# Optimization experiments

Hardware: AMD Instinct MI355X
Metric: run time of the kernel (lower is better)

The kernel has to match this reference:

```python
import jax, jax.numpy as jnp
import numpy as np

EPS = 1e-5
NUM_HEADS = 16
NUM_KV_HEADS = 4
HEAD_DIM = 64
TOP_K = 2


def _layer_norm(x, w, b):
    m = jnp.mean(x, axis=-1, keepdims=True)
    v = jnp.mean((x - m) ** 2, axis=-1, keepdims=True)
    return (x - m) * jax.lax.rsqrt(v + EPS) * w + b


def setup_inputs() -> dict:
    key = jax.random.key(0)
    ks = jax.random.split(key, 8)
    S, B, H = 2048, 1, 1024
    E, F = 8, 4096
    q_per_kv = NUM_HEADS // NUM_KV_HEADS
    qkv_out = NUM_KV_HEADS * (q_per_kv + 2) * HEAD_DIM  # 1536

    def w(k, shape, scale=0.02):
        return jax.random.normal(k, shape, dtype=jnp.float32) * scale

    return {
        "hidden_states": jax.random.normal(ks[0], (S, B, H), dtype=jnp.float32),
        "ln1_weight": jnp.ones((H,), jnp.float32),
        "ln1_bias": jnp.zeros((H,), jnp.float32),
        "ln2_weight": jnp.ones((H,), jnp.float32),
        "ln2_bias": jnp.zeros((H,), jnp.float32),
        "qkv_weight": w(ks[1], (qkv_out, H)),
        "proj_weight": w(ks[2], (H, H)),
        "router_weight": w(ks[3], (H, E)),
        "moe_w1": w(ks[4], (E, H, F)),
        "moe_w2": w(ks[5], (E, F, H)),
    }


def reference(hidden_states, ln1_weight, ln1_bias, ln2_weight, ln2_bias,
              qkv_weight, proj_weight, router_weight, moe_w1, moe_w2):
    S, B, H = hidden_states.shape
    D = HEAD_DIM
    Hq, Hkv = NUM_HEADS, NUM_KV_HEADS
    g = Hq // Hkv                      # queries per kv head (GQA group)
    scale = 1.0 / np.sqrt(D)

    # ---- attention block ----
    ln1_out = _layer_norm(hidden_states, ln1_weight, ln1_bias)
    qkv = ln1_out @ qkv_weight.T                      # [S,B,Hkv*(g+2)*D]
    qkv = qkv.reshape(S, B, Hkv, (g + 2) * D)
    q = qkv[..., : g * D].reshape(S, B, Hq, D)        # [S,B,Hq,D]
    k = qkv[..., g * D : (g + 1) * D]                 # [S,B,Hkv,D]
    v = qkv[..., (g + 1) * D :]                       # [S,B,Hkv,D]

    # cp_size == 1 -> Ulysses all-to-alls are identity
    q_bf = q.transpose(1, 2, 0, 3).reshape(B, Hkv, g, S, D)  # [B,Hkv,g,S,D]
    k_bf = k.transpose(1, 2, 0, 3)                           # [B,Hkv,S,D]
    v_bf = v.transpose(1, 2, 0, 3)

    scores = jnp.einsum("bkgsd,bktd->bkgst", q_bf, k_bf) * scale
    causal = jnp.tril(jnp.ones((S, S), dtype=bool))
    scores = jnp.where(causal, scores, jnp.float32(-1e30))
    probs = jax.nn.softmax(scores, axis=-1)
    attn = jnp.einsum("bkgst,bktd->bkgsd", probs, v_bf)      # [B,Hkv,g,S,D]
    attn = attn.reshape(B, Hq, S, D).transpose(2, 0, 1, 3).reshape(S, B, Hq * D)

    proj_out = attn @ proj_weight.T
    hidden_after_attn = hidden_states + proj_out

    # ---- MoE block ----
    ln2_out = _layer_norm(hidden_after_attn, ln2_weight, ln2_bias)
    x = ln2_out.reshape(-1, H)                        # [T,H]
    T = x.shape[0]

    logits = x @ router_weight                        # [T,E] (fp32)
    rprobs = jax.nn.softmax(logits, axis=-1)
    top_p, top_i = jax.lax.top_k(rprobs, TOP_K)       # [T,k]
    top_p = top_p / jnp.sum(top_p, axis=-1, keepdims=True)

    # ep_size == 1: dispatch/sort/all-to-all are a pure permutation; compute
    # each expert densely over all tokens, then gather the routed outputs
    # (identical math to sort+grouped-GEMM+unsort).
    fc1 = jnp.einsum("th,ehf->etf", x, moe_w1)        # [E,T,F]
    act = jax.nn.gelu(fc1, approximate=False)
    y = jnp.einsum("etf,efh->eth", act, moe_w2)       # [E,T,H]

    tok = jnp.arange(T)[:, None]                      # [T,1]
    gathered = y[top_i, tok, :]                       # [T,k,H]
    moe_out = jnp.sum(gathered * top_p[..., None], axis=1)  # [T,H]

    return hidden_after_attn + moe_out.reshape(S, B, H)
```

## Files before the change

kernel.cpp:

```cpp
#include <hip/hip_runtime.h>
#include <cstdint>
#include <cstddef>

typedef unsigned short u16;
typedef __attribute__((ext_vector_type(8))) short bf16x8;
typedef __attribute__((ext_vector_type(4))) float f32x4;

#define MFMA16(a, b, c) __builtin_amdgcn_mfma_f32_16x16x32_bf16((a), (b), (c), 0, 0, 0)

__device__ __forceinline__ u16 f2bf(float f) {
  uint32_t u = __builtin_bit_cast(uint32_t, f);
  u += 0x7fffu + ((u >> 16) & 1u);
  return (u16)(u >> 16);
}
__device__ __forceinline__ float bf2f(u16 h) {
  uint32_t u = ((uint32_t)h) << 16;
  return __builtin_bit_cast(float, u);
}

__device__ __forceinline__ void gload_lds16(const void* g, void* l) {
  __builtin_amdgcn_global_load_lds(
      (const __attribute__((address_space(1))) uint32_t*)g,
      (__attribute__((address_space(3))) uint32_t*)l, 16, 0, 0);
}

template<bool WRITE_LO, bool WRITE_F32>
__launch_bounds__(256)
__global__ void ln_kernel(const float* __restrict__ in,
                          const float* __restrict__ w, const float* __restrict__ b,
                          u16* __restrict__ out_hi, u16* __restrict__ out_lo,
                          float* __restrict__ out_f32)
{
  int row = blockIdx.x;
  int tid = threadIdx.x;
  const float* x = in + (size_t)row * 1024;
  float4 v = *(const float4*)(x + tid * 4);
  float s  = v.x + v.y + v.z + v.w;
  float s2 = v.x*v.x + v.y*v.y + v.z*v.z + v.w*v.w;
  #pragma unroll
  for (int d = 1; d < 64; d <<= 1) { s += __shfl_xor(s, d); s2 += __shfl_xor(s2, d); }
  __shared__ float red[2][4];
  int wid = tid >> 6;
  if ((tid & 63) == 0) { red[0][wid] = s; red[1][wid] = s2; }
  __syncthreads();
  s  = red[0][0] + red[0][1] + red[0][2] + red[0][3];
  s2 = red[1][0] + red[1][1] + red[1][2] + red[1][3];
  float mean = s * (1.0f / 1024.0f);
  float var  = s2 * (1.0f / 1024.0f) - mean * mean;
  float rstd = rsqrtf(var + 1e-5f);
  float vv[4] = {v.x, v.y, v.z, v.w};
  #pragma unroll
  for (int j = 0; j < 4; ++j) {
    int c = tid * 4 + j;
    float y = (vv[j] - mean) * rstd * w[c] + b[c];
    size_t idx = (size_t)row * 1024 + c;
    u16 hb = f2bf(y);
    out_hi[idx] = hb;
    if (WRITE_LO)  out_lo[idx] = f2bf(y - bf2f(hb));
    if (WRITE_F32) out_f32[idx] = y;
  }
}

__global__ void convert_split_kernel(const float* __restrict__ in,
                                     u16* __restrict__ hi, u16* __restrict__ lo, int n4)
{
  int i = blockIdx.x * blockDim.x + threadIdx.x;
  if (i >= n4) return;
  float4 v = *(const float4*)(in + (size_t)i * 4);
  float a[4] = {v.x, v.y, v.z, v.w};
  u16 hh[4], ll[4];
  #pragma unroll
  for (int j = 0; j < 4; ++j) {
    hh[j] = f2bf(a[j]);
    ll[j] = f2bf(a[j] - bf2f(hh[j]));
  }
  uint2 hp, lp;
  hp.x = (uint32_t)hh[0] | ((uint32_t)hh[1] << 16);
  hp.y = (uint32_t)hh[2] | ((uint32_t)hh[3] << 16);
  lp.x = (uint32_t)ll[0] | ((uint32_t)ll[1] << 16);
  lp.y = (uint32_t)ll[2] | ((uint32_t)ll[3] << 16);
  *(uint2*)(hi + (size_t)i * 4) = hp;
  *(uint2*)(lo + (size_t)i * 4) = lp;
}

__global__ void transpose_convert_kernel(const float* __restrict__ in, u16* __restrict__ out,
                                         int R, int C)
{
  __shared__ float t[32][33];
  size_t ebase = (size_t)blockIdx.z * R * C;
  int c0 = blockIdx.x * 32, r0 = blockIdx.y * 32;
  int tx = threadIdx.x, ty = threadIdx.y;
  #pragma unroll
  for (int i = 0; i < 4; ++i)
    t[ty + 8*i][tx] = in[ebase + (size_t)(r0 + ty + 8*i) * C + (c0 + tx)];
  __syncthreads();
  #pragma unroll
  for (int i = 0; i < 4; ++i)
    out[ebase + (size_t)(c0 + ty + 8*i) * R + (r0 + tx)] = f2bf(t[tx][ty + 8*i]);
}

__global__ void vtrans_kernel(const u16* __restrict__ qkv, u16* __restrict__ vT)
{
  __shared__ u16 t[32][34];
  int kvh = blockIdx.z;
  int s0 = blockIdx.x * 32, d0 = blockIdx.y * 32;
  int tx = threadIdx.x, ty = threadIdx.y;
  #pragma unroll
  for (int i = 0; i < 4; ++i)
    t[ty + 8*i][tx] = qkv[(size_t)(s0 + ty + 8*i) * 1536 + kvh * 384 + 320 + d0 + tx];
  __syncthreads();
  #pragma unroll
  for (int i = 0; i < 4; ++i)
    vT[((size_t)kvh * 64 + d0 + ty + 8*i) * 2048 + (s0 + tx)] = t[tx][ty + 8*i];
}

template<int MODE, bool SPLIT>
__launch_bounds__(256, SPLIT ? 2 : 4)
__global__ void gemm_kernel(const u16* __restrict__ Ahi, const u16* __restrict__ Alo,
                            const u16* __restrict__ Bhi, const u16* __restrict__ Blo,
                            int N, int K,
                            u16* __restrict__ Cb_hi, u16* __restrict__ Cb_lo,
                            float* __restrict__ Cf, const float* __restrict__ resid,
                            const int* __restrict__ tok_of_pair,
                            const int* __restrict__ counts, const int* __restrict__ prefix)
{
  int bn = blockIdx.x, bm = blockIdx.y;
  int row_base = 0;
  int count = 1 << 30;
  int kbeg = 0, kend = K;
  if constexpr (MODE >= 2) {
    int e = blockIdx.z;
    count = counts[e];
    if (bm * 128 >= count) return;
    row_base = prefix[e];
    Bhi += (size_t)e * N * K;
  }
  if constexpr (MODE == 3) {
    int s = bn >> 3;
    bn &= 7;
    int kc = K >> 2;
    kbeg = s * kc; kend = kbeg + kc;
    Cf += (size_t)s * 4096 * 1024;
  }
  __shared__ u16 As[2][SPLIT ? 2 : 1][128 * 32];
  __shared__ u16 Bs[2][SPLIT ? 2 : 1][128 * 32];

  int tid = threadIdx.x;
  int lane = tid & 63;
  int lo16 = lane & 15, hi4 = lane >> 4;
  int wid = tid >> 6, wr = wid >> 1, wc = wid & 1;

  const u16* gA[2][2];
  const u16* gB[2][2];
  int eidx[2];
  #pragma unroll
  for (int q = 0; q < 2; ++q) {
    int el = (q * 256 + tid) * 8;
    int r = el >> 5, c = el & 31;
    eidx[q] = el;
    if constexpr (MODE == 2) {
      int lim = count - bm * 128 - 1;
      int lr = r < lim ? r : lim;
      int token = tok_of_pair[row_base + bm * 128 + lr];
      gA[q][0] = Ahi + (size_t)token * K + c;
    } else if constexpr (MODE == 3) {
      int lim = count - bm * 128 - 1;
      int lr = r < lim ? r : lim;
      gA[q][0] = Ahi + (size_t)(row_base + bm * 128 + lr) * K + c;
    } else {
      gA[q][0] = Ahi + (size_t)(bm * 128 + r) * K + c;
      if constexpr (SPLIT) gA[q][1] = Alo + (size_t)(bm * 128 + r) * K + c;
    }
    gB[q][0] = Bhi + (size_t)(bn * 128 + r) * K + c;
    if constexpr (SPLIT) gB[q][1] = Blo + (size_t)(bn * 128 + r) * K + c;
  }

  auto stage = [&](int buf, int k0) {
    #pragma unroll
    for (int q = 0; q < 2; ++q) {
      gload_lds16(gA[q][0] + k0, &As[buf][0][eidx[q]]);
      gload_lds16(gB[q][0] + k0, &Bs[buf][0][eidx[q]]);
      if constexpr (SPLIT) {
        gload_lds16(gA[q][1] + k0, &As[buf][1][eidx[q]]);
        gload_lds16(gB[q][1] + k0, &Bs[buf][1][eidx[q]]);
      }
    }
  };

  const f32x4 zf = {0.f, 0.f, 0.f, 0.f};
  f32x4 acc[4][4];
  #pragma unroll
  for (int m = 0; m < 4; ++m)
    #pragma unroll
    for (int n = 0; n < 4; ++n) acc[m][n] = zf;

  stage(0, kbeg);
  __syncthreads();

  int cur = 0;
  for (int k0 = kbeg; k0 < kend; k0 += 32, cur ^= 1) {
    if (k0 + 32 < kend) stage(cur ^ 1, k0 + 32);

    bf16x8 a0[4], b0[4], a1[4], b1[4];
    #pragma unroll
    for (int m = 0; m < 4; ++m)
      a0[m] = *(const bf16x8*)&As[cur][0][(wr * 64 + m * 16 + lo16) * 32 + hi4 * 8];
    #pragma unroll
    for (int n = 0; n < 4; ++n)
      b0[n] = *(const bf16x8*)&Bs[cur][0][(wc * 64 + n * 16 + lo16) * 32 + hi4 * 8];
    if constexpr (SPLIT) {
      #pragma unroll
      for (int m = 0; m < 4; ++m)
        a1[m] = *(const bf16x8*)&As[cur][1][(wr * 64 + m * 16 + lo16) * 32 + hi4 * 8];
      #pragma unroll
      for (int n = 0; n < 4; ++n)
        b1[n] = *(const bf16x8*)&Bs[cur][1][(wc * 64 + n * 16 + lo16) * 32 + hi4 * 8];
    }
    #pragma unroll
    for (int m = 0; m < 4; ++m)
      #pragma unroll
      for (int n = 0; n < 4; ++n) {
        acc[m][n] = MFMA16(a0[m], b0[n], acc[m][n]);
        if constexpr (SPLIT) {
          acc[m][n] = MFMA16(a0[m], b1[n], acc[m][n]);
          acc[m][n] = MFMA16(a1[m], b0[n], acc[m][n]);
        }
      }
    __syncthreads();
  }

  #pragma unroll
  for (int m = 0; m < 4; ++m)
    #pragma unroll
    for (int n = 0; n < 4; ++n)
      #pragma unroll
      for (int r = 0; r < 4; ++r) {
        int lr = wr * 64 + m * 16 + hi4 * 4 + r;
        int col = bn * 128 + wc * 64 + n * 16 + lo16;
        float v = acc[m][n][r];
        if constexpr (MODE == 0) {
          size_t idx = (size_t)(bm * 128 + lr) * N + col;
          u16 hb = f2bf(v);
          Cb_hi[idx] = hb;
          Cb_lo[idx] = f2bf(v - bf2f(hb));
        } else if constexpr (MODE == 1) {
          size_t idx = (size_t)(bm * 128 + lr) * N + col;
          Cf[idx] = v + resid[idx];
        } else if constexpr (MODE == 2) {
          if (bm * 128 + lr < count) {
            size_t idx = (size_t)(row_base + bm * 128 + lr) * N + col;
            float g = 0.5f * v * (1.0f + erff(v * 0.70710678118654752f));
            Cb_hi[idx] = f2bf(g);
          }
        } else {
          if (bm * 128 + lr < count) {
            size_t idx = (size_t)(row_base + bm * 128 + lr) * N + col;
            Cf[idx] = v;
          }
        }
      }
}

__launch_bounds__(256)
__global__ void attn_kernel(const u16* __restrict__ qkv_hi, const u16* __restrict__ qkv_lo,
                            const u16* __restrict__ vT_hi, const u16* __restrict__ vT_lo,
                            u16* __restrict__ out_hi, u16* __restrict__ out_lo)
{
  int qb = (int)(gridDim.x - 1 - blockIdx.x);
  int h = blockIdx.y;
  int kvh = h >> 2, gi = h & 3;
  int tid = threadIdx.x;
  int lane = tid & 63;
  int w = tid >> 6;
  int lo16 = lane & 15, hi4 = lane >> 4;
  int q0w = qb * 64 + w * 16;
  int qoff = kvh * 384 + gi * 64;
  int koff = kvh * 384 + 256;

  __shared__ u16 Ks[2][64 * 64];
  __shared__ u16 Vs[2][64 * 64];
  __shared__ u16 Ps[2][4][16 * 72];

  bf16x8 qf[2][2];
  {
    const u16* ph = qkv_hi + (size_t)(q0w + lo16) * 1536 + qoff + hi4 * 8;
    const u16* pl = qkv_lo + (size_t)(q0w + lo16) * 1536 + qoff + hi4 * 8;
    qf[0][0] = *(const bf16x8*)ph;  qf[0][1] = *(const bf16x8*)(ph + 32);
    qf[1][0] = *(const bf16x8*)pl;  qf[1][1] = *(const bf16x8*)(pl + 32);
  }

  const f32x4 zf = {0.f, 0.f, 0.f, 0.f};
  float m_r[4], l_r[4];
  f32x4 o[4];
  #pragma unroll
  for (int r = 0; r < 4; ++r) { m_r[r] = -INFINITY; l_r[r] = 0.f; }
  #pragma unroll
  for (int n = 0; n < 4; ++n) o[n] = zf;

  int qrow[4];
  #pragma unroll
  for (int r = 0; r < 4; ++r) qrow[r] = q0w + hi4 * 4 + r;

  for (int t = 0; t <= qb; ++t) {
    int kv0 = t * 64;
    __syncthreads();
    #pragma unroll
    for (int it = 0; it < 2; ++it) {
      int u = it * 256 + tid;
      int row = u >> 3, ch = u & 7;
      int d = ((ch ^ (row & 7))) * 8;
      *(uint4*)&Ks[0][row * 64 + d] = *(const uint4*)(qkv_hi + (size_t)(kv0 + row) * 1536 + koff + ch * 8);
      *(uint4*)&Ks[1][row * 64 + d] = *(const uint4*)(qkv_lo + (size_t)(kv0 + row) * 1536 + koff + ch * 8);
      *(uint4*)&Vs[0][row * 64 + d] = *(const uint4*)(vT_hi + ((size_t)kvh * 64 + row) * 2048 + kv0 + ch * 8);
      *(uint4*)&Vs[1][row * 64 + d] = *(const uint4*)(vT_lo + ((size_t)kvh * 64 + row) * 2048 + kv0 + ch * 8);
    }
    __syncthreads();

    f32x4 sc[4];
    #pragma unroll
    for (int c2 = 0; c2 < 4; ++c2) {
      sc[c2] = zf;
      int krow = c2 * 16 + lo16;
      const u16* kb  = &Ks[0][krow * 64];
      const u16* kbl = &Ks[1][krow * 64];
      bf16x8 kh0 = *(const bf16x8*)&kb [((hi4    ) ^ (krow & 7)) * 8];
      bf16x8 kh1 = *(const bf16x8*)&kb [((hi4 + 4) ^ (krow & 7)) * 8];
      bf16x8 kl0 = *(const bf16x8*)&kbl[((hi4    ) ^ (krow & 7)) * 8];
      bf16x8 kl1 = *(const bf16x8*)&kbl[((hi4 + 4) ^ (krow & 7)) * 8];
      sc[c2] = MFMA16(qf[0][0], kh0, sc[c2]);
      sc[c2] = MFMA16(qf[0][1], kh1, sc[c2]);
      sc[c2] = MFMA16(qf[0][0], kl0, sc[c2]);
      sc[c2] = MFMA16(qf[0][1], kl1, sc[c2]);
      sc[c2] = MFMA16(qf[1][0], kh0, sc[c2]);
      sc[c2] = MFMA16(qf[1][1], kh1, sc[c2]);
    }

    float tmax[4] = {-INFINITY, -INFINITY, -INFINITY, -INFINITY};
    #pragma unroll
    for (int c2 = 0; c2 < 4; ++c2) {
      int kv = kv0 + c2 * 16 + lo16;
      #pragma unroll
      for (int r = 0; r < 4; ++r) {
        float sv = sc[c2][r] * 0.125f;
        if (kv > qrow[r]) sv = -1e30f;
        sc[c2][r] = sv;
        tmax[r] = fmaxf(tmax[r], sv);
      }
    }
    #pragma unroll
    for (int d = 1; d < 16; d <<= 1)
      #pragma unroll
      for (int r = 0; r < 4; ++r)
        tmax[r] = fmaxf(tmax[r], __shfl_xor(tmax[r], d));
    float rs[4], rowsum[4];
    #pragma unroll
    for (int r = 0; r < 4; ++r) {
      float mn = fmaxf(m_r[r], tmax[r]);
      rs[r] = __expf(m_r[r] - mn);
      m_r[r] = mn;
      rowsum[r] = 0.f;
    }
    #pragma unroll
    for (int c2 = 0; c2 < 4; ++c2)
      #pragma unroll
      for (int r = 0; r < 4; ++r) {
        float pv = __expf(sc[c2][r] - m_r[r]);
        sc[c2][r] = pv;
        rowsum[r] += pv;
      }
    #pragma unroll
    for (int d = 1; d < 16; d <<= 1)
      #pragma unroll
      for (int r = 0; r < 4; ++r)
        rowsum[r] += __shfl_xor(rowsum[r], d);
    #pragma unroll
    for (int r = 0; r < 4; ++r) l_r[r] = l_r[r] * rs[r] + rowsum[r];
    #pragma unroll
    for (int n = 0; n < 4; ++n)
      #pragma unroll
      for (int r = 0; r < 4; ++r) o[n][r] *= rs[r];

    #pragma unroll
    for (int c2 = 0; c2 < 4; ++c2)
      #pragma unroll
      for (int r = 0; r < 4; ++r) {
        float pv = sc[c2][r];
        u16 ph = f2bf(pv);
        int pidx = (hi4 * 4 + r) * 72 + c2 * 16 + lo16;
        Ps[0][w][pidx] = ph;
        Ps[1][w][pidx] = f2bf(pv - bf2f(ph));
      }
    __syncthreads();

    #pragma unroll
    for (int k2 = 0; k2 < 2; ++k2) {
      bf16x8 pah = *(const bf16x8*)&Ps[0][w][lo16 * 72 + k2 * 32 + hi4 * 8];
      bf16x8 pal = *(const bf16x8*)&Ps[1][w][lo16 * 72 + k2 * 32 + hi4 * 8];
      #pragma unroll
      for (int n = 0; n < 4; ++n) {
        int vrow = n * 16 + lo16;
        bf16x8 vh = *(const bf16x8*)&Vs[0][vrow * 64 + (((k2 * 4 + hi4) ^ (vrow & 7))) * 8];
        bf16x8 vl = *(const bf16x8*)&Vs[1][vrow * 64 + (((k2 * 4 + hi4) ^ (vrow & 7))) * 8];
        o[n] = MFMA16(pah, vh, o[n]);
        o[n] = MFMA16(pah, vl, o[n]);
        o[n] = MFMA16(pal, vh, o[n]);
      }
    }
  }

  #pragma unroll
  for (int n = 0; n < 4; ++n)
    #pragma unroll
    for (int r = 0; r < 4; ++r) {
      float v = o[n][r] / l_r[r];
      size_t idx = (size_t)(q0w + hi4 * 4 + r) * 1024 + h * 64 + n * 16 + lo16;
      u16 hb = f2bf(v);
      out_hi[idx] = hb;
      out_lo[idx] = f2bf(v - bf2f(hb));
    }
}

__launch_bounds__(64)
__global__ void router_kernel(const float* __restrict__ x, const float* __restrict__ rw,
                              int* __restrict__ counts, int* __restrict__ esel,
                              int* __restrict__ slotsel, float* __restrict__ wsel)
{
  int t = blockIdx.x;
  int l = threadIdx.x;
  float acc[8] = {0.f, 0.f, 0.f, 0.f, 0.f, 0.f, 0.f, 0.f};
  const float* xr = x + (size_t)t * 1024;
  for (int hh = l; hh < 1024; hh += 64) {
    float xv = xr[hh];
    const float* wp = rw + hh * 8;
    #pragma unroll
    for (int e = 0; e < 8; ++e) acc[e] = fmaf(xv, wp[e], acc[e]);
  }
  #pragma unroll
  for (int e = 0; e < 8; ++e)
    #pragma unroll
    for (int d = 1; d < 64; d <<= 1) acc[e] += __shfl_xor(acc[e], d);
  if (l == 0) {
    int e1 = 0;
    #pragma unroll
    for (int e = 1; e < 8; ++e) if (acc[e] > acc[e1]) e1 = e;
    int e2 = -1;
    #pragma unroll
    for (int e = 0; e < 8; ++e) {
      if (e == e1) continue;
      if (e2 < 0 || acc[e] > acc[e2]) e2 = e;
    }
    float p1 = 1.0f / (1.0f + expf(acc[e2] - acc[e1]));
    float p2 = 1.0f - p1;
    int s1 = atomicAdd(&counts[e1], 1);
    int s2 = atomicAdd(&counts[e2], 1);
    esel[t * 2] = e1; esel[t * 2 + 1] = e2;
    slotsel[t * 2] = s1; slotsel[t * 2 + 1] = s2;
    wsel[t * 2] = p1; wsel[t * 2 + 1] = p2;
  }
}

__global__ void build_lists_kernel(const int* __restrict__ counts, int* __restrict__ prefix,
                                   const int* __restrict__ esel, const int* __restrict__ slotsel,
                                   int* __restrict__ tok_of_pair, int* __restrict__ pair_idx)
{
  __shared__ int pfx[8];
  if (threadIdx.x == 0) {
    int a = 0;
    for (int e = 0; e < 8; ++e) { pfx[e] = a; prefix[e] = a; a += counts[e]; }
  }
  __syncthreads();
  for (int t = threadIdx.x; t < 2048; t += 256) {
    #pragma unroll
    for (int k = 0; k < 2; ++k) {
      int e = esel[t * 2 + k];
      int row = pfx[e] + slotsel[t * 2 + k];
      tok_of_pair[row] = t;
      pair_idx[t * 2 + k] = row;
    }
  }
}

__launch_bounds__(256)
__global__ void final_kernel(const float* __restrict__ hattn, const float* __restrict__ y,
                             const int* __restrict__ pair_idx, const float* __restrict__ wsel,
                             float* __restrict__ out)
{
  int t = blockIdx.x;
  int c = threadIdx.x * 4;
  int p0 = pair_idx[t * 2], p1 = pair_idx[t * 2 + 1];
  float w0 = wsel[t * 2], w1 = wsel[t * 2 + 1];
  float4 a = *(const float4*)(hattn + (size_t)t * 1024 + c);
  float y0x = 0.f, y0y = 0.f, y0z = 0.f, y0w = 0.f;
  float y1x = 0.f, y1y = 0.f, y1z = 0.f, y1w = 0.f;
  #pragma unroll
  for (int s = 0; s < 4; ++s) {
    const float* base = y + (size_t)s * 4096 * 1024;
    float4 v0 = *(const float4*)(base + (size_t)p0 * 1024 + c);
    float4 v1 = *(const float4*)(base + (size_t)p1 * 1024 + c);
    y0x += v0.x; y0y += v0.y; y0z += v0.z; y0w += v0.w;
    y1x += v1.x; y1y += v1.y; y1z += v1.z; y1w += v1.w;
  }
  float4 r;
  r.x = a.x + w0 * y0x + w1 * y1x;
  r.y = a.y + w0 * y0y + w1 * y1y;
  r.z = a.z + w0 * y0z + w1 * y1z;
  r.w = a.w + w0 * y0w + w1 * y1w;
  *(float4*)(out + (size_t)t * 1024 + c) = r;
}

extern "C" void kernel_launch(void* const* d_in, const int* in_sizes, int n_in,
                              void* d_out, int out_size, void* d_ws, size_t ws_size,
                              hipStream_t stream)
{
  const float* hidden   = (const float*)d_in[0];
  const float* ln1_w    = (const float*)d_in[1];
  const float* ln1_b    = (const float*)d_in[2];
  const float* ln2_w    = (const float*)d_in[3];
  const float* ln2_b    = (const float*)d_in[4];
  const float* qkv_w    = (const float*)d_in[5];
  const float* proj_w   = (const float*)d_in[6];
  const float* router_w = (const float*)d_in[7];
  const float* moe_w1   = (const float*)d_in[8];
  const float* moe_w2   = (const float*)d_in[9];
  float* out = (float*)d_out;

  char* ws = (char*)d_ws;
  size_t off = 0;
  auto alloc = [&](size_t bytes) -> void* {
    void* p = (void*)(ws + off);
    off += (bytes + 255) & ~(size_t)255;
    return p;
  };

  u16* wT      = (u16*)alloc(8ull * 4096 * 1024 * 2);
  float* hattn = (float*)alloc(2048ull * 1024 * 4);
  u16* x_hi    = (u16*)alloc(2048ull * 1024 * 2);
  u16* act     = (u16*)alloc(4096ull * 4096 * 2);
  float* ybuf  = (float*)alloc(4ull * 4096 * 1024 * 4);

  {
    char* ov = (char*)ybuf;
    size_t oo = 0;
    auto oalloc = [&](size_t bytes) -> void* {
      void* p = (void*)(ov + oo);
      oo += (bytes + 255) & ~(size_t)255;
      return p;
    };
    (void)oalloc;
  }
  char* ov = (char*)ybuf;
  size_t oo = 0;
  auto oalloc = [&](size_t bytes) -> void* {
    void* p = (void*)(ov + oo);
    oo += (bytes + 255) & ~(size_t)255;
    return p;
  };
  u16* ln1_hi  = (u16*)oalloc(2048ull * 1024 * 2);
  u16* ln1_lo  = (u16*)oalloc(2048ull * 1024 * 2);
  u16* qw_hi   = (u16*)oalloc(1536ull * 1024 * 2);
  u16* qw_lo   = (u16*)oalloc(1536ull * 1024 * 2);
  u16* pw_hi   = (u16*)oalloc(1024ull * 1024 * 2);
  u16* pw_lo   = (u16*)oalloc(1024ull * 1024 * 2);
  u16* qkv_hi  = (u16*)oalloc(2048ull * 1536 * 2);
  u16* qkv_lo  = (u16*)oalloc(2048ull * 1536 * 2);
  u16* vt_hi   = (u16*)oalloc(4ull * 64 * 2048 * 2);
  u16* vt_lo   = (u16*)oalloc(4ull * 64 * 2048 * 2);
  u16* at_hi   = (u16*)oalloc(2048ull * 1024 * 2);
  u16* at_lo   = (u16*)oalloc(2048ull * 1024 * 2);
  float* x_f32 = (float*)oalloc(2048ull * 1024 * 4);

  int* counts  = (int*)alloc(8 * 4);
  int* prefix  = (int*)alloc(8 * 4);
  int* esel    = (int*)alloc(2048ull * 2 * 4);
  int* slotsel = (int*)alloc(2048ull * 2 * 4);
  int* topair  = (int*)alloc(4096ull * 4);
  int* pairidx = (int*)alloc(2048ull * 2 * 4);
  float* wsel  = (float*)alloc(2048ull * 2 * 4);

  hipMemsetAsync(counts, 0, 8 * 4, stream);

  ln_kernel<true, false><<<2048, 256, 0, stream>>>(hidden, ln1_w, ln1_b, ln1_hi, ln1_lo, nullptr);

  convert_split_kernel<<<1536, 256, 0, stream>>>(qkv_w, qw_hi, qw_lo, 1536 * 1024 / 4);
  convert_split_kernel<<<1024, 256, 0, stream>>>(proj_w, pw_hi, pw_lo, 1024 * 1024 / 4);

  gemm_kernel<0, true><<<dim3(12, 16, 1), 256, 0, stream>>>(
      ln1_hi, ln1_lo, qw_hi, qw_lo, 1536, 1024,
      qkv_hi, qkv_lo, nullptr, nullptr, nullptr, nullptr, nullptr);

  vtrans_kernel<<<dim3(64, 2, 4), dim3(32, 8), 0, stream>>>(qkv_hi, vt_hi);
  vtrans_kernel<<<dim3(64, 2, 4), dim3(32, 8), 0, stream>>>(qkv_lo, vt_lo);

  attn_kernel<<<dim3(32, 16), 256, 0, stream>>>(qkv_hi, qkv_lo, vt_hi, vt_lo, at_hi, at_lo);

  gemm_kernel<1, true><<<dim3(8, 16, 1), 256, 0, stream>>>(
      at_hi, at_lo, pw_hi, pw_lo, 1024, 1024,
      nullptr, nullptr, hattn, hidden, nullptr, nullptr, nullptr);

  ln_kernel<false, true><<<2048, 256, 0, stream>>>(hattn, ln2_w, ln2_b, x_hi, nullptr, x_f32);

  router_kernel<<<2048, 64, 0, stream>>>(x_f32, router_w, counts, esel, slotsel, wsel);
  build_lists_kernel<<<1, 256, 0, stream>>>(counts, prefix, esel, slotsel, topair, pairidx);

  transpose_convert_kernel<<<dim3(128, 32, 8), dim3(32, 8), 0, stream>>>(moe_w1, wT, 1024, 4096);

  gemm_kernel<2, false><<<dim3(32, 16, 8), 256, 0, stream>>>(
      x_hi, nullptr, wT, nullptr, 4096, 1024,
      act, nullptr, nullptr, nullptr, topair, counts, prefix);

  transpose_convert_kernel<<<dim3(32, 128, 8), dim3(32, 8), 0, stream>>>(moe_w2, wT, 4096, 1024);

  gemm_kernel<3, false><<<dim3(32, 16, 8), 256, 0, stream>>>(
      act, nullptr, wT, nullptr, 1024, 4096,
      nullptr, nullptr, ybuf, nullptr, topair, counts, prefix);

  final_kernel<<<2048, 256, 0, stream>>>(hattn, ybuf, pairidx, wsel, out);
}
```

Baseline: 526.3 us.

## Pair causal query blocks per workgroup and prefetch next K/V tile into registers

Each attention workgroup now processes two query blocks (31-p and p), so every block does the same total causal work. The two blocks share each loaded K/V tile, and the grid is halved to 256 workgroups. The next K/V tile is loaded into registers while the current one is being computed, hiding global-load latency, and s_setprio raises wave priority around the MFMA sections. In exchange, each thread holds two Q/O states plus the prefetch buffers, which raises register pressure and may lower occupancy; the per-warp P-buffer barrier is also dropped.

```diff
diff --git a/kernel.cpp b/kernel.cpp
--- a/kernel.cpp
+++ b/kernel.cpp
@@ -261,163 +261,209 @@
       }
 }
 
+struct QState {
+  bf16x8 qf[2][2];
+  f32x4 o[4];
+  float m_r[4], l_r[4];
+  int qrow[4];
+};
+
+__device__ __forceinline__ void qstate_init(QState& S,
+    const u16* qkv_hi, const u16* qkv_lo, int q0w, int qoff, int lo16, int hi4)
+{
+  const u16* ph = qkv_hi + (size_t)(q0w + lo16) * 1536 + qoff + hi4 * 8;
+  const u16* pl = qkv_lo + (size_t)(q0w + lo16) * 1536 + qoff + hi4 * 8;
+  S.qf[0][0] = *(const bf16x8*)ph;  S.qf[0][1] = *(const bf16x8*)(ph + 32);
+  S.qf[1][0] = *(const bf16x8*)pl;  S.qf[1][1] = *(const bf16x8*)(pl + 32);
+  const f32x4 zf = {0.f, 0.f, 0.f, 0.f};
+  #pragma unroll
+  for (int r = 0; r < 4; ++r) { S.m_r[r] = -INFINITY; S.l_r[r] = 0.f; S.qrow[r] = q0w + hi4 * 4 + r; }
+  #pragma unroll
+  for (int n = 0; n < 4; ++n) S.o[n] = zf;
+}
+
+__device__ __forceinline__ void attn_tile(QState& S, int kv0,
+    const u16* Ks0, const u16* Ks1, const u16* Vs0, const u16* Vs1,
+    u16* Ps0, u16* Ps1, int lo16, int hi4)
+{
+  const f32x4 zf = {0.f, 0.f, 0.f, 0.f};
+  f32x4 sc[4];
+  __builtin_amdgcn_s_setprio(1);
+  #pragma unroll
+  for (int c2 = 0; c2 < 4; ++c2) {
+    sc[c2] = zf;
+    int krow = c2 * 16 + lo16;
+    const u16* kb  = &Ks0[krow * 64];
+    const u16* kbl = &Ks1[krow * 64];
+    bf16x8 kh0 = *(const bf16x8*)&kb [((hi4    ) ^ (krow & 7)) * 8];
+    bf16x8 kh1 = *(const bf16x8*)&kb [((hi4 + 4) ^ (krow & 7)) * 8];
+    bf16x8 kl0 = *(const bf16x8*)&kbl[((hi4    ) ^ (krow & 7)) * 8];
+    bf16x8 kl1 = *(const bf16x8*)&kbl[((hi4 + 4) ^ (krow & 7)) * 8];
+    sc[c2] = MFMA16(S.qf[0][0], kh0, sc[c2]);
+    sc[c2] = MFMA16(S.qf[0][1], kh1, sc[c2]);
+    sc[c2] = MFMA16(S.qf[0][0], kl0, sc[c2]);
+    sc[c2] = MFMA16(S.qf[0][1], kl1, sc[c2]);
+    sc[c2] = MFMA16(S.qf[1][0], kh0, sc[c2]);
+    sc[c2] = MFMA16(S.qf[1][1], kh1, sc[c2]);
+  }
+  __builtin_amdgcn_s_setprio(0);
+
+  float tmax[4] = {-INFINITY, -INFINITY, -INFINITY, -INFINITY};
+  #pragma unroll
+  for (int c2 = 0; c2 < 4; ++c2) {
+    int kv = kv0 + c2 * 16 + lo16;
+    #pragma unroll
+    for (int r = 0; r < 4; ++r) {
+      float sv = sc[c2][r] * 0.125f;
+      if (kv > S.qrow[r]) sv = -1e30f;
+      sc[c2][r] = sv;
+      tmax[r] = fmaxf(tmax[r], sv);
+    }
+  }
+  #pragma unroll
+  for (int d = 1; d < 16; d <<= 1)
+    #pragma unroll
+    for (int r = 0; r < 4; ++r)
+      tmax[r] = fmaxf(tmax[r], __shfl_xor(tmax[r], d));
+  float rs[4], rowsum[4];
+  #pragma unroll
+  for (int r = 0; r < 4; ++r) {
+    float mn = fmaxf(S.m_r[r], tmax[r]);
+    rs[r] = __expf(S.m_r[r] - mn);
+    S.m_r[r] = mn;
+    rowsum[r] = 0.f;
+  }
+  #pragma unroll
+  for (int c2 = 0; c2 < 4; ++c2)
+    #pragma unroll
+    for (int r = 0; r < 4; ++r) {
+      float pv = __expf(sc[c2][r] - S.m_r[r]);
+      sc[c2][r] = pv;
+      rowsum[r] += pv;
+    }
+  #pragma unroll
+  for (int d = 1; d < 16; d <<= 1)
+    #pragma unroll
+    for (int r = 0; r < 4; ++r)
+      rowsum[r] += __shfl_xor(rowsum[r], d);
+  #pragma unroll
+  for (int r = 0; r < 4; ++r) S.l_r[r] = S.l_r[r] * rs[r] + rowsum[r];
+  #pragma unroll
+  for (int n = 0; n < 4; ++n)
+    #pragma unroll
+    for (int r = 0; r < 4; ++r) S.o[n][r] *= rs[r];
+
+  #pragma unroll
+  for (int c2 = 0; c2 < 4; ++c2)
+    #pragma unroll
+    for (int r = 0; r < 4; ++r) {
+      float pv = sc[c2][r];
+      u16 ph = f2bf(pv);
+      int pidx = (hi4 * 4 + r) * 72 + c2 * 16 + lo16;
+      Ps0[pidx] = ph;
+      Ps1[pidx] = f2bf(pv - bf2f(ph));
+    }
+
+  __builtin_amdgcn_s_setprio(1);
+  #pragma unroll
+  for (int k2 = 0; k2 < 2; ++k2) {
+    bf16x8 pah = *(const bf16x8*)&Ps0[lo16 * 72 + k2 * 32 + hi4 * 8];
+    bf16x8 pal = *(const bf16x8*)&Ps1[lo16 * 72 + k2 * 32 + hi4 * 8];
+    #pragma unroll
+    for (int n = 0; n < 4; ++n) {
+      int vrow = n * 16 + lo16;
+      bf16x8 vh = *(const bf16x8*)&Vs0[vrow * 64 + (((k2 * 4 + hi4) ^ (vrow & 7))) * 8];
+      bf16x8 vl = *(const bf16x8*)&Vs1[vrow * 64 + (((k2 * 4 + hi4) ^ (vrow & 7))) * 8];
+      S.o[n] = MFMA16(pah, vh, S.o[n]);
+      S.o[n] = MFMA16(pah, vl, S.o[n]);
+      S.o[n] = MFMA16(pal, vh, S.o[n]);
+    }
+  }
+  __builtin_amdgcn_s_setprio(0);
+}
+
+__device__ __forceinline__ void qstate_out(QState& S, int q0w, int h,
+    u16* out_hi, u16* out_lo, int lo16, int hi4)
+{
+  #pragma unroll
+  for (int n = 0; n < 4; ++n)
+    #pragma unroll
+    for (int r = 0; r < 4; ++r) {
+      float v = S.o[n][r] / S.l_r[r];
+      size_t idx = (size_t)(q0w + hi4 * 4 + r) * 1024 + h * 64 + n * 16 + lo16;
+      u16 hb = f2bf(v);
+      out_hi[idx] = hb;
+      out_lo[idx] = f2bf(v - bf2f(hb));
+    }
+}
+
 __launch_bounds__(256)
 __global__ void attn_kernel(const u16* __restrict__ qkv_hi, const u16* __restrict__ qkv_lo,
                             const u16* __restrict__ vT_hi, const u16* __restrict__ vT_lo,
                             u16* __restrict__ out_hi, u16* __restrict__ out_lo)
 {
-  int qb = (int)(gridDim.x - 1 - blockIdx.x);
+  int p = blockIdx.x;
   int h = blockIdx.y;
   int kvh = h >> 2, gi = h & 3;
   int tid = threadIdx.x;
   int lane = tid & 63;
   int w = tid >> 6;
   int lo16 = lane & 15, hi4 = lane >> 4;
-  int q0w = qb * 64 + w * 16;
+  int qbA = 31 - p, qbB = p;
+  int q0A = qbA * 64 + w * 16;
+  int q0B = qbB * 64 + w * 16;
   int qoff = kvh * 384 + gi * 64;
   int koff = kvh * 384 + 256;
 
   __shared__ u16 Ks[2][64 * 64];
   __shared__ u16 Vs[2][64 * 64];
   __shared__ u16 Ps[2][4][16 * 72];
-
-  bf16x8 qf[2][2];
-  {
-    const u16* ph = qkv_hi + (size_t)(q0w + lo16) * 1536 + qoff + hi4 * 8;
-    const u16* pl = qkv_lo + (size_t)(q0w + lo16) * 1536 + qoff + hi4 * 8;
-    qf[0][0] = *(const bf16x8*)ph;  qf[0][1] = *(const bf16x8*)(ph + 32);
-    qf[1][0] = *(const bf16x8*)pl;  qf[1][1] = *(const bf16x8*)(pl + 32);
-  }
-
-  const f32x4 zf = {0.f, 0.f, 0.f, 0.f};
-  float m_r[4], l_r[4];
-  f32x4 o[4];
-  #pragma unroll
-  for (int r = 0; r < 4; ++r) { m_r[r] = -INFINITY; l_r[r] = 0.f; }
-  #pragma unroll
-  for (int n = 0; n < 4; ++n) o[n] = zf;
-
-  int qrow[4];
-  #pragma unroll
-  for (int r = 0; r < 4; ++r) qrow[r] = q0w + hi4 * 4 + r;
-
-  for (int t = 0; t <= qb; ++t) {
+  u16* Ps0 = &Ps[0][w][0];
+  u16* Ps1 = &Ps[1][w][0];
+
+  QState SA, SB;
+  qstate_init(SA, qkv_hi, qkv_lo, q0A, qoff, lo16, hi4);
+  qstate_init(SB, qkv_hi, qkv_lo, q0B, qoff, lo16, hi4);
+
+  int prow[2], pch[2];
+  #pragma unroll
+  for (int it = 0; it < 2; ++it) {
+    int u = it * 256 + tid;
+    prow[it] = u >> 3; pch[it] = u & 7;
+  }
+  uint4 rk0[2], rk1[2], rv0[2], rv1[2];
+  auto issue = [&](int kv0) {
+    #pragma unroll
+    for (int it = 0; it < 2; ++it) {
+      rk0[it] = *(const uint4*)(qkv_hi + (size_t)(kv0 + prow[it]) * 1536 + koff + pch[it] * 8);
+      rk1[it] = *(const uint4*)(qkv_lo + (size_t)(kv0 + prow[it]) * 1536 + koff + pch[it] * 8);
+      rv0[it] = *(const uint4*)(vT_hi + ((size_t)kvh * 64 + prow[it]) * 2048 + kv0 + pch[it] * 8);
+      rv1[it] = *(const uint4*)(vT_lo + ((size_t)kvh * 64 + prow[it]) * 2048 + kv0 + pch[it] * 8);
+    }
+  };
+  issue(0);
+
+  for (int t = 0; t <= qbA; ++t) {
     int kv0 = t * 64;
     __syncthreads();
     #pragma unroll
     for (int it = 0; it < 2; ++it) {
-      int u = it * 256 + tid;
-      int row = u >> 3, ch = u & 7;
-      int d = ((ch ^ (row & 7))) * 8;
-      *(uint4*)&Ks[0][row * 64 + d] = *(const uint4*)(qkv_hi + (size_t)(kv0 + row) * 1536 + koff + ch * 8);
-      *(uint4*)&Ks[1][row * 64 + d] = *(const uint4*)(qkv_lo + (size_t)(kv0 + row) * 1536 + koff + ch * 8);
-      *(uint4*)&Vs[0][row * 64 + d] = *(const uint4*)(vT_hi + ((size_t)kvh * 64 + row) * 2048 + kv0 + ch * 8);
-      *(uint4*)&Vs[1][row * 64 + d] = *(const uint4*)(vT_lo + ((size_t)kvh * 64 + row) * 2048 + kv0 + ch * 8);
-    }
+      int d = (pch[it] ^ (prow[it] & 7)) * 8;
+      *(uint4*)&Ks[0][prow[it] * 64 + d] = rk0[it];
+      *(uint4*)&Ks[1][prow[it] * 64 + d] = rk1[it];
+      *(uint4*)&Vs[0][prow[it] * 64 + d] = rv0[it];
+      *(uint4*)&Vs[1][prow[it] * 64 + d] = rv1[it];
+    }
+    if (t < qbA) issue(kv0 + 64);
     __syncthreads();
 
-    f32x4 sc[4];
-    #pragma unroll
-    for (int c2 = 0; c2 < 4; ++c2) {
-      sc[c2] = zf;
-      int krow = c2 * 16 + lo16;
-      const u16* kb  = &Ks[0][krow * 64];
-      const u16* kbl = &Ks[1][krow * 64];
-      bf16x8 kh0 = *(const bf16x8*)&kb [((hi4    ) ^ (krow & 7)) * 8];
-      bf16x8 kh1 = *(const bf16x8*)&kb [((hi4 + 4) ^ (krow & 7)) * 8];
-      bf16x8 kl0 = *(const bf16x8*)&kbl[((hi4    ) ^ (krow & 7)) * 8];
-      bf16x8 kl1 = *(const bf16x8*)&kbl[((hi4 + 4) ^ (krow & 7)) * 8];
-      sc[c2] = MFMA16(qf[0][0], kh0, sc[c2]);
-      sc[c2] = MFMA16(qf[0][1], kh1, sc[c2]);
-      sc[c2] = MFMA16(qf[0][0], kl0, sc[c2]);
-      sc[c2] = MFMA16(qf[0][1], kl1, sc[c2]);
-      sc[c2] = MFMA16(qf[1][0], kh0, sc[c2]);
-      sc[c2] = MFMA16(qf[1][1], kh1, sc[c2]);
-    }
-
-    float tmax[4] = {-INFINITY, -INFINITY, -INFINITY, -INFINITY};
-    #pragma unroll
-    for (int c2 = 0; c2 < 4; ++c2) {
-      int kv = kv0 + c2 * 16 + lo16;
-      #pragma unroll
-      for (int r = 0; r < 4; ++r) {
-        float sv = sc[c2][r] * 0.125f;
-        if (kv > qrow[r]) sv = -1e30f;
-        sc[c2][r] = sv;
-        tmax[r] = fmaxf(tmax[r], sv);
-      }
-    }
-    #pragma unroll
-    for (int d = 1; d < 16; d <<= 1)
-      #pragma unroll
-      for (int r = 0; r < 4; ++r)
-        tmax[r] = fmaxf(tmax[r], __shfl_xor(tmax[r], d));
-    float rs[4], rowsum[4];
-    #pragma unroll
-    for (int r = 0; r < 4; ++r) {
-      float mn = fmaxf(m_r[r], tmax[r]);
-      rs[r] = __expf(m_r[r] - mn);
-      m_r[r] = mn;
-      rowsum[r] = 0.f;
-    }
-    #pragma unroll
-    for (int c2 = 0; c2 < 4; ++c2)
-      #pragma unroll
-      for (int r = 0; r < 4; ++r) {
-        float pv = __expf(sc[c2][r] - m_r[r]);
-        sc[c2][r] = pv;
-        rowsum[r] += pv;
-      }
-    #pragma unroll
-    for (int d = 1; d < 16; d <<= 1)
-      #pragma unroll
-      for (int r = 0; r < 4; ++r)
-        rowsum[r] += __shfl_xor(rowsum[r], d);
-    #pragma unroll
-    for (int r = 0; r < 4; ++r) l_r[r] = l_r[r] * rs[r] + rowsum[r];
-    #pragma unroll
-    for (int n = 0; n < 4; ++n)
-      #pragma unroll
-      for (int r = 0; r < 4; ++r) o[n][r] *= rs[r];
-
-    #pragma unroll
-    for (int c2 = 0; c2 < 4; ++c2)
-      #pragma unroll
-      for (int r = 0; r < 4; ++r) {
-        float pv = sc[c2][r];
-        u16 ph = f2bf(pv);
-        int pidx = (hi4 * 4 + r) * 72 + c2 * 16 + lo16;
-        Ps[0][w][pidx] = ph;
-        Ps[1][w][pidx] = f2bf(pv - bf2f(ph));
-      }
-    __syncthreads();
-
-    #pragma unroll
-    for (int k2 = 0; k2 < 2; ++k2) {
-      bf16x8 pah = *(const bf16x8*)&Ps[0][w][lo16 * 72 + k2 * 32 + hi4 * 8];
-      bf16x8 pal = *(const bf16x8*)&Ps[1][w][lo16 * 72 + k2 * 32 + hi4 * 8];
-      #pragma unroll
-      for (int n = 0; n < 4; ++n) {
-        int vrow = n * 16 + lo16;
-        bf16x8 vh = *(const bf16x8*)&Vs[0][vrow * 64 + (((k2 * 4 + hi4) ^ (vrow & 7))) * 8];
-        bf16x8 vl = *(const bf16x8*)&Vs[1][vrow * 64 + (((k2 * 4 + hi4) ^ (vrow & 7))) * 8];
-        o[n] = MFMA16(pah, vh, o[n]);
-        o[n] = MFMA16(pah, vl, o[n]);
-        o[n] = MFMA16(pal, vh, o[n]);
-      }
-    }
-  }
-
-  #pragma unroll
-  for (int n = 0; n < 4; ++n)
-    #pragma unroll
-    for (int r = 0; r < 4; ++r) {
-      float v = o[n][r] / l_r[r];
-      size_t idx = (size_t)(q0w + hi4 * 4 + r) * 1024 + h * 64 + n * 16 + lo16;
-      u16 hb = f2bf(v);
-      out_hi[idx] = hb;
-      out_lo[idx] = f2bf(v - bf2f(hb));
-    }
+    attn_tile(SA, kv0, Ks[0], Ks[1], Vs[0], Vs[1], Ps0, Ps1, lo16, hi4);
+    if (t <= qbB)
+      attn_tile(SB, kv0, Ks[0], Ks[1], Vs[0], Vs[1], Ps0, Ps1, lo16, hi4);
+  }
+
+  qstate_out(SA, q0A, h, out_hi, out_lo, lo16, hi4);
+  qstate_out(SB, q0B, h, out_hi, out_lo, lo16, hi4);
 }
 
 __launch_bounds__(64)
@@ -538,16 +584,6 @@
   u16* act     = (u16*)alloc(4096ull * 4096 * 2);
   float* ybuf  = (float*)alloc(4ull * 4096 * 1024 * 4);
 
-  {
-    char* ov = (char*)ybuf;
-    size_t oo = 0;
-    auto oalloc = [&](size_t bytes) -> void* {
-      void* p = (void*)(ov + oo);
-      oo += (bytes + 255) & ~(size_t)255;
-      return p;
-    };
-    (void)oalloc;
-  }
   char* ov = (char*)ybuf;
   size_t oo = 0;
   auto oalloc = [&](size_t bytes) -> void* {
@@ -591,7 +627,7 @@
   vtrans_kernel<<<dim3(64, 2, 4), dim3(32, 8), 0, stream>>>(qkv_hi, vt_hi);
   vtrans_kernel<<<dim3(64, 2, 4), dim3(32, 8), 0, stream>>>(qkv_lo, vt_lo);
 
-  attn_kernel<<<dim3(32, 16), 256, 0, stream>>>(qkv_hi, qkv_lo, vt_hi, vt_lo, at_hi, at_lo);
+  attn_kernel<<<dim3(16, 16), 256, 0, stream>>>(qkv_hi, qkv_lo, vt_hi, vt_lo, at_hi, at_lo);
 
   gemm_kernel<1, true><<<dim3(8, 16, 1), 256, 0, stream>>>(
       at_hi, at_lo, pw_hi, pw_lo, 1024, 1024,
```

After: 601.4 us. 1.14x slower.
